# Kernel tuning notes

Measured on AMD Instinct MI355X. Metric: run time of the kernel, lower is better.

## Reference

```python
import jax, jax.numpy as jnp
import numpy as np

DIM = 512
CTX_DIM = 1024
NUM_HEADS = 8
HEAD_DIM = DIM // NUM_HEADS
SCALE = DIM ** (-0.5)  # module uses full dim, not head_dim


def setup_inputs() -> dict:
    key = jax.random.key(0)
    k1, k2, k3, k4, k5 = jax.random.split(key, 5)
    B, NQ, NK = 4, 1024, 2048
    q = jax.random.normal(k1, (B, NQ, DIM), dtype=jnp.float32)
    context = jax.random.normal(k2, (B, NK, CTX_DIM), dtype=jnp.float32)
    # Linear weights stored as [in, out] so projection is x @ W (no bias).
    Wq = jax.random.normal(k3, (DIM, DIM), dtype=jnp.float32) * (DIM ** -0.5)
    Wk = jax.random.normal(k4, (CTX_DIM, DIM), dtype=jnp.float32) * (CTX_DIM ** -0.5)
    Wv = jax.random.normal(k5, (CTX_DIM, DIM), dtype=jnp.float32) * (CTX_DIM ** -0.5)
    return {"q": q, "context": context, "Wq": Wq, "Wk": Wk, "Wv": Wv}


def reference(q, context, Wq, Wk, Wv):
    B, NQ, _ = q.shape
    # Projections
    qh = (q @ Wq).reshape(B, NQ, NUM_HEADS, HEAD_DIM)          # [B,Nq,H,D]
    kh = (context @ Wk).reshape(B, -1, NUM_HEADS, HEAD_DIM)     # [B,Nk,H,D]
    vh = (context @ Wv).reshape(B, -1, NUM_HEADS, HEAD_DIM)     # [B,Nk,H,D]
    # Scores and softmax (dropout is identity in eval / reference mode)
    attn_scores = jnp.einsum("bqhd,bkhd->bhqk", qh, kh) * SCALE
    attn_weights = jax.nn.softmax(attn_scores, axis=-1)         # [B,H,Nq,Nk]
    # Weighted sum of values, merge heads back
    ctx = jnp.einsum("bhqk,bkhd->bqhd", attn_weights, vh)
    context_vec = ctx.reshape(B, NQ, NUM_HEADS * HEAD_DIM)      # [B,Nq,dim]
    return context_vec, attn_weights
```

## Files before the change

### kernel.cpp

```cpp
#include <hip/hip_runtime.h>
#include <hip/hip_bf16.h>

#define B_ 4
#define NQ_ 1024
#define NK_ 2048
#define DIM_ 512
#define CTX_ 1024
#define NH_ 8
#define HD_ 64
static constexpr float SCALE_ = 0.04419417382415922f;

typedef short bf16x8 __attribute__((ext_vector_type(8)));
typedef float f32x4 __attribute__((ext_vector_type(4)));

__device__ __forceinline__ unsigned f2u(float f) { union { float f; unsigned u; } v; v.f = f; return v.u; }

__device__ __forceinline__ bf16x8 pack8(float4 lo, float4 hi) {
  union { unsigned u[4]; bf16x8 v; } r;
  r.u[0] = __builtin_amdgcn_perm(f2u(lo.y), f2u(lo.x), 0x07060302u);
  r.u[1] = __builtin_amdgcn_perm(f2u(lo.w), f2u(lo.z), 0x07060302u);
  r.u[2] = __builtin_amdgcn_perm(f2u(hi.y), f2u(hi.x), 0x07060302u);
  r.u[3] = __builtin_amdgcn_perm(f2u(hi.w), f2u(hi.z), 0x07060302u);
  return r.v;
}

__device__ __forceinline__ unsigned short f2bf_rne(float f) {
  unsigned u = f2u(f);
  u += 0x7fffu + ((u >> 16) & 1u);
  return (unsigned short)(u >> 16);
}

__global__ __launch_bounds__(256) void transpose_w(
    const float* __restrict__ Wq, const float* __restrict__ Wk,
    const float* __restrict__ Wv, unsigned short* __restrict__ Wt) {
  int mat = blockIdx.z;
  const float* W; unsigned short* T; int K;
  if (mat == 0)      { W = Wq; T = Wt;                         K = DIM_; }
  else if (mat == 1) { W = Wk; T = Wt + DIM_*DIM_;             K = CTX_; }
  else               { W = Wv; T = Wt + DIM_*DIM_ + DIM_*CTX_; K = CTX_; }
  int k0 = blockIdx.x * 64;
  if (k0 >= K) return;
  int n0 = blockIdx.y * 64;
  __shared__ unsigned short tl[64][64];
  int tid = threadIdx.x;
  {
    int nb = (tid & 15) * 4;
    int rbase = tid >> 4;
    #pragma unroll
    for (int p = 0; p < 4; ++p) {
      int kr = rbase + p * 16;
      float4 v = *(const float4*)(W + (size_t)(k0 + kr) * DIM_ + n0 + nb);
      int ck = kr >> 3, ko = kr & 7;
      tl[nb + 0][((ck ^ ((nb + 0) & 7)) << 3) | ko] = (unsigned short)(f2u(v.x) >> 16);
      tl[nb + 1][((ck ^ ((nb + 1) & 7)) << 3) | ko] = (unsigned short)(f2u(v.y) >> 16);
      tl[nb + 2][((ck ^ ((nb + 2) & 7)) << 3) | ko] = (unsigned short)(f2u(v.z) >> 16);
      tl[nb + 3][((ck ^ ((nb + 3) & 7)) << 3) | ko] = (unsigned short)(f2u(v.w) >> 16);
    }
  }
  __syncthreads();
  {
    int nr = tid >> 2, cc = tid & 3;
    #pragma unroll
    for (int p = 0; p < 2; ++p) {
      int c = cc + p * 4;
      bf16x8 v = *(const bf16x8*)&tl[nr][(c ^ (nr & 7)) << 3];
      *(bf16x8*)(T + (size_t)(n0 + nr) * K + k0 + c * 8) = v;
    }
  }
}

template<int TRANS>
__global__ __launch_bounds__(256) void gemm_proj(
    const float* __restrict__ A, const unsigned short* __restrict__ Wt,
    unsigned short* __restrict__ C, int M, int K) {
  int tid = threadIdx.x, lane = tid & 63, wid = tid >> 6;
  int m0 = blockIdx.x * 128 + (wid >> 1) * 64;
  int n0 = blockIdx.y * 128 + (wid & 1) * 64;
  int rl = lane & 15, ch = (lane >> 4) * 8;
  const float* aptr = A + (size_t)(m0 + rl) * K + ch;
  const unsigned short* bptr = Wt + (size_t)(n0 + rl) * K + ch;
  f32x4 acc[4][4] = {};
  for (int k0 = 0; k0 < K; k0 += 32) {
    bf16x8 af[4], bfr[4];
    #pragma unroll
    for (int i = 0; i < 4; ++i) {
      const float* p = aptr + (size_t)i * 16 * K + k0;
      float4 lo = *(const float4*)p;
      float4 hi = *(const float4*)(p + 4);
      af[i] = pack8(lo, hi);
    }
    #pragma unroll
    for (int j = 0; j < 4; ++j)
      bfr[j] = *(const bf16x8*)(bptr + (size_t)j * 16 * K + k0);
    #pragma unroll
    for (int i = 0; i < 4; ++i)
      #pragma unroll
      for (int j = 0; j < 4; ++j)
        acc[i][j] = __builtin_amdgcn_mfma_f32_16x16x32_bf16(af[i], bfr[j], acc[i][j], 0, 0, 0);
  }
  int rq = (lane >> 4) * 4, cn = lane & 15;
  #pragma unroll
  for (int i = 0; i < 4; ++i)
    #pragma unroll
    for (int j = 0; j < 4; ++j)
      #pragma unroll
      for (int r = 0; r < 4; ++r) {
        int row = m0 + i * 16 + rq + r;
        int col = n0 + j * 16 + cn;
        unsigned short v = f2bf_rne(acc[i][j][r]);
        if (TRANS) {
          int b = row >> 11, k = row & 2047;
          int h = col >> 6, d = col & 63;
          C[((size_t)(b * NH_ + h) * HD_ + d) * NK_ + k] = v;
        } else {
          C[(size_t)row * DIM_ + col] = v;
        }
      }
}

__global__ __launch_bounds__(256) void attn_fwd(
    const unsigned short* __restrict__ Qh, const unsigned short* __restrict__ Kh,
    const unsigned short* __restrict__ Vt, float* __restrict__ outO,
    float* __restrict__ outW) {
  int bid = blockIdx.x;
  int qt = bid & 15, h = (bid >> 4) & 7, b = bid >> 7;
  int tid = threadIdx.x, lane = tid & 63, wid = tid >> 6;
  int q0 = qt * 64 + wid * 16;
  int rl = lane & 15, ch = (lane >> 4) * 8, rq = (lane >> 4) * 4;
  __shared__ unsigned short Plds[4][16][40];

  const unsigned short* qbase = Qh + (size_t)(b * NQ_ + q0 + rl) * DIM_ + h * HD_;
  bf16x8 aq0 = *(const bf16x8*)(qbase + ch);
  bf16x8 aq1 = *(const bf16x8*)(qbase + 32 + ch);

  const unsigned short* kbase = Kh + (size_t)(b * NK_ + rl) * DIM_ + h * HD_;

  float ps[4] = {0.f, 0.f, 0.f, 0.f};
  #pragma unroll 4
  for (int kt = 0; kt < NK_ / 16; ++kt) {
    const unsigned short* kp = kbase + (size_t)kt * 16 * DIM_;
    bf16x8 bk0 = *(const bf16x8*)(kp + ch);
    bf16x8 bk1 = *(const bf16x8*)(kp + 32 + ch);
    f32x4 s = {};
    s = __builtin_amdgcn_mfma_f32_16x16x32_bf16(aq0, bk0, s, 0, 0, 0);
    s = __builtin_amdgcn_mfma_f32_16x16x32_bf16(aq1, bk1, s, 0, 0, 0);
    #pragma unroll
    for (int r = 0; r < 4; ++r) ps[r] += __expf(s[r] * SCALE_);
  }
  #pragma unroll
  for (int m = 1; m < 16; m <<= 1)
    #pragma unroll
    for (int r = 0; r < 4; ++r) ps[r] += __shfl_xor(ps[r], m);
  float inv[4];
  #pragma unroll
  for (int r = 0; r < 4; ++r) inv[r] = 1.0f / ps[r];

  f32x4 accO[4] = {};
  float* wbase = outW + (size_t)((b * NH_ + h) * NQ_ + q0 + rq) * NK_;
  for (int kc = 0; kc < NK_ / 32; ++kc) {
    #pragma unroll
    for (int t = 0; t < 2; ++t) {
      int kt = kc * 2 + t;
      const unsigned short* kp = kbase + (size_t)kt * 16 * DIM_;
      bf16x8 bk0 = *(const bf16x8*)(kp + ch);
      bf16x8 bk1 = *(const bf16x8*)(kp + 32 + ch);
      f32x4 s = {};
      s = __builtin_amdgcn_mfma_f32_16x16x32_bf16(aq0, bk0, s, 0, 0, 0);
      s = __builtin_amdgcn_mfma_f32_16x16x32_bf16(aq1, bk1, s, 0, 0, 0);
      #pragma unroll
      for (int r = 0; r < 4; ++r) {
        float p = __expf(s[r] * SCALE_) * inv[r];
        wbase[(size_t)r * NK_ + kt * 16 + rl] = p;
        Plds[wid][rq + r][t * 16 + rl] = (unsigned short)(f2u(p) >> 16);
      }
    }
    bf16x8 ap = *(const bf16x8*)&Plds[wid][rl][ch];
    #pragma unroll
    for (int dt = 0; dt < 4; ++dt) {
      const unsigned short* vp =
          Vt + ((size_t)(b * NH_ + h) * HD_ + dt * 16 + rl) * NK_ + kc * 32 + ch;
      bf16x8 bv = *(const bf16x8*)vp;
      accO[dt] = __builtin_amdgcn_mfma_f32_16x16x32_bf16(ap, bv, accO[dt], 0, 0, 0);
    }
  }
  float* obase = outO + (size_t)(b * NQ_ + q0 + rq) * DIM_ + h * HD_;
  #pragma unroll
  for (int dt = 0; dt < 4; ++dt)
    #pragma unroll
    for (int r = 0; r < 4; ++r)
      obase[(size_t)r * DIM_ + dt * 16 + rl] = accO[dt][r];
}

extern "C" void kernel_launch(void* const* d_in, const int* in_sizes, int n_in,
                              void* d_out, int out_size, void* d_ws, size_t ws_size,
                              hipStream_t stream) {
  (void)in_sizes; (void)n_in; (void)out_size; (void)ws_size;
  const float* q   = (const float*)d_in[0];
  const float* ctx = (const float*)d_in[1];
  const float* Wq  = (const float*)d_in[2];
  const float* Wk  = (const float*)d_in[3];
  const float* Wv  = (const float*)d_in[4];

  unsigned short* Wt = (unsigned short*)d_ws;
  unsigned short* Qh = Wt + 1310720;
  unsigned short* Kh = Qh + 2097152;
  unsigned short* Vt = Kh + 4194304;
  float* outO = (float*)d_out;
  float* outW = outO + (size_t)B_ * NQ_ * DIM_;

  transpose_w<<<dim3(16, 8, 3), 256, 0, stream>>>(Wq, Wk, Wv, Wt);
  gemm_proj<0><<<dim3(32, 4), 256, 0, stream>>>(q,   Wt,                  Qh, 4096, DIM_);
  gemm_proj<0><<<dim3(64, 4), 256, 0, stream>>>(ctx, Wt + 262144,         Kh, 8192, CTX_);
  gemm_proj<1><<<dim3(64, 4), 256, 0, stream>>>(ctx, Wt + 262144 + 524288, Vt, 8192, CTX_);
  attn_fwd<<<dim3(512), 256, 0, stream>>>(Qh, Kh, Vt, outO, outW);
}
```

Baseline: 564.5 us.

## Fuse K and V projections into one GEMM and shrink projection tiles

Replaces the templated projection GEMM with a Q-only kernel and a fused K/V kernel. The fused kernel reads each context fragment once and feeds both the Wk and Wv MFMAs, removing one full pass over the fp32 context tensor. Tiles shrink from 128x128 to 64x64 per block, which raises the block count for better CU occupancy but lowers per-wave operand reuse. The transposed V store stays scattered.

```diff
diff --git a/kernel.cpp b/kernel.cpp
--- a/kernel.cpp
+++ b/kernel.cpp
@@ -69,53 +69,72 @@
   }
 }
 
-template<int TRANS>
-__global__ __launch_bounds__(256) void gemm_proj(
+__global__ __launch_bounds__(256) void gemm_q(
     const float* __restrict__ A, const unsigned short* __restrict__ Wt,
-    unsigned short* __restrict__ C, int M, int K) {
+    unsigned short* __restrict__ C) {
   int tid = threadIdx.x, lane = tid & 63, wid = tid >> 6;
-  int m0 = blockIdx.x * 128 + (wid >> 1) * 64;
-  int n0 = blockIdx.y * 128 + (wid & 1) * 64;
+  int m0 = blockIdx.x * 64 + wid * 16;
+  int n0 = blockIdx.y * 64;
   int rl = lane & 15, ch = (lane >> 4) * 8;
-  const float* aptr = A + (size_t)(m0 + rl) * K + ch;
-  const unsigned short* bptr = Wt + (size_t)(n0 + rl) * K + ch;
-  f32x4 acc[4][4] = {};
-  for (int k0 = 0; k0 < K; k0 += 32) {
-    bf16x8 af[4], bfr[4];
-    #pragma unroll
-    for (int i = 0; i < 4; ++i) {
-      const float* p = aptr + (size_t)i * 16 * K + k0;
-      float4 lo = *(const float4*)p;
-      float4 hi = *(const float4*)(p + 4);
-      af[i] = pack8(lo, hi);
-    }
-    #pragma unroll
-    for (int j = 0; j < 4; ++j)
-      bfr[j] = *(const bf16x8*)(bptr + (size_t)j * 16 * K + k0);
-    #pragma unroll
-    for (int i = 0; i < 4; ++i)
-      #pragma unroll
-      for (int j = 0; j < 4; ++j)
-        acc[i][j] = __builtin_amdgcn_mfma_f32_16x16x32_bf16(af[i], bfr[j], acc[i][j], 0, 0, 0);
-  }
-  int rq = (lane >> 4) * 4, cn = lane & 15;
-  #pragma unroll
-  for (int i = 0; i < 4; ++i)
-    #pragma unroll
-    for (int j = 0; j < 4; ++j)
-      #pragma unroll
-      for (int r = 0; r < 4; ++r) {
-        int row = m0 + i * 16 + rq + r;
-        int col = n0 + j * 16 + cn;
-        unsigned short v = f2bf_rne(acc[i][j][r]);
-        if (TRANS) {
-          int b = row >> 11, k = row & 2047;
-          int h = col >> 6, d = col & 63;
-          C[((size_t)(b * NH_ + h) * HD_ + d) * NK_ + k] = v;
-        } else {
-          C[(size_t)row * DIM_ + col] = v;
-        }
-      }
+  const float* aptr = A + (size_t)(m0 + rl) * DIM_ + ch;
+  const unsigned short* bptr = Wt + (size_t)(n0 + rl) * DIM_ + ch;
+  f32x4 acc[4] = {};
+  #pragma unroll 4
+  for (int k0 = 0; k0 < DIM_; k0 += 32) {
+    float4 lo = *(const float4*)(aptr + k0);
+    float4 hi = *(const float4*)(aptr + k0 + 4);
+    bf16x8 af = pack8(lo, hi);
+    #pragma unroll
+    for (int j = 0; j < 4; ++j) {
+      bf16x8 bfr = *(const bf16x8*)(bptr + (size_t)j * 16 * DIM_ + k0);
+      acc[j] = __builtin_amdgcn_mfma_f32_16x16x32_bf16(af, bfr, acc[j], 0, 0, 0);
+    }
+  }
+  int rq = (lane >> 4) * 4;
+  #pragma unroll
+  for (int j = 0; j < 4; ++j)
+    #pragma unroll
+    for (int r = 0; r < 4; ++r)
+      C[(size_t)(m0 + rq + r) * DIM_ + n0 + j * 16 + rl] = f2bf_rne(acc[j][r]);
+}
+
+__global__ __launch_bounds__(256) void gemm_kv(
+    const float* __restrict__ A, const unsigned short* __restrict__ Wtk,
+    const unsigned short* __restrict__ Wtv, unsigned short* __restrict__ Kh,
+    unsigned short* __restrict__ Vt) {
+  int tid = threadIdx.x, lane = tid & 63, wid = tid >> 6;
+  int m0 = blockIdx.x * 64 + wid * 16;
+  int n0 = blockIdx.y * 64;
+  int rl = lane & 15, ch = (lane >> 4) * 8;
+  const float* aptr = A + (size_t)(m0 + rl) * CTX_ + ch;
+  const unsigned short* bkp = Wtk + (size_t)(n0 + rl) * CTX_ + ch;
+  const unsigned short* bvp = Wtv + (size_t)(n0 + rl) * CTX_ + ch;
+  f32x4 accK[4] = {}, accV[4] = {};
+  #pragma unroll 2
+  for (int k0 = 0; k0 < CTX_; k0 += 32) {
+    float4 lo = *(const float4*)(aptr + k0);
+    float4 hi = *(const float4*)(aptr + k0 + 4);
+    bf16x8 af = pack8(lo, hi);
+    #pragma unroll
+    for (int j = 0; j < 4; ++j) {
+      bf16x8 bk = *(const bf16x8*)(bkp + (size_t)j * 16 * CTX_ + k0);
+      accK[j] = __builtin_amdgcn_mfma_f32_16x16x32_bf16(af, bk, accK[j], 0, 0, 0);
+      bf16x8 bv = *(const bf16x8*)(bvp + (size_t)j * 16 * CTX_ + k0);
+      accV[j] = __builtin_amdgcn_mfma_f32_16x16x32_bf16(af, bv, accV[j], 0, 0, 0);
+    }
+  }
+  int rq = (lane >> 4) * 4;
+  #pragma unroll
+  for (int j = 0; j < 4; ++j)
+    #pragma unroll
+    for (int r = 0; r < 4; ++r) {
+      int row = m0 + rq + r;
+      int col = n0 + j * 16 + rl;
+      Kh[(size_t)row * DIM_ + col] = f2bf_rne(accK[j][r]);
+      int b = row >> 11, kk = row & 2047;
+      int h = col >> 6, d = col & 63;
+      Vt[((size_t)(b * NH_ + h) * HD_ + d) * NK_ + kk] = f2bf_rne(accV[j][r]);
+    }
 }
 
 __global__ __launch_bounds__(256) void attn_fwd(
@@ -209,8 +228,7 @@
   float* outW = outO + (size_t)B_ * NQ_ * DIM_;
 
   transpose_w<<<dim3(16, 8, 3), 256, 0, stream>>>(Wq, Wk, Wv, Wt);
-  gemm_proj<0><<<dim3(32, 4), 256, 0, stream>>>(q,   Wt,                  Qh, 4096, DIM_);
-  gemm_proj<0><<<dim3(64, 4), 256, 0, stream>>>(ctx, Wt + 262144,         Kh, 8192, CTX_);
-  gemm_proj<1><<<dim3(64, 4), 256, 0, stream>>>(ctx, Wt + 262144 + 524288, Vt, 8192, CTX_);
+  gemm_q<<<dim3(64, 8), 256, 0, stream>>>(q, Wt, Qh);
+  gemm_kv<<<dim3(128, 8), 256, 0, stream>>>(ctx, Wt + 262144, Wt + 786432, Kh, Vt);
   attn_fwd<<<dim3(512), 256, 0, stream>>>(Qh, Kh, Vt, outO, outW);
 }
```

Result: slower. 615.0 us (+8.9%).

## Split attention denominator and main pass across key chunks for more parallelism

Applied to the files above, without the earlier changes.

Moves the softmax-denominator pass into its own kernel, which launches many small blocks over query tiles and key chunks, followed by a reduction kernel. The main pass splits the key dimension across the four waves of each block, writes partial outputs to workspace, and sums them in a combine kernel. A fused fallback is used when the workspace is too small. The aim is to fill the GPU better than the original 512-block launch, at the cost of extra launches and partial-output traffic.

```diff
diff --git a/kernel.cpp b/kernel.cpp
--- a/kernel.cpp
+++ b/kernel.cpp
@@ -118,26 +118,24 @@
       }
 }
 
-__global__ __launch_bounds__(256) void attn_fwd(
+__global__ __launch_bounds__(256) void attn_denom(
     const unsigned short* __restrict__ Qh, const unsigned short* __restrict__ Kh,
-    const unsigned short* __restrict__ Vt, float* __restrict__ outO,
-    float* __restrict__ outW) {
+    float* __restrict__ dnm_part) {
   int bid = blockIdx.x;
-  int qt = bid & 15, h = (bid >> 4) & 7, b = bid >> 7;
+  int kchi = bid & 3, qt = (bid >> 2) & 63, h = (bid >> 8) & 7, b = bid >> 11;
   int tid = threadIdx.x, lane = tid & 63, wid = tid >> 6;
-  int q0 = qt * 64 + wid * 16;
+  int kc = kchi * 4 + wid;
+  int q0 = qt * 16;
   int rl = lane & 15, ch = (lane >> 4) * 8, rq = (lane >> 4) * 4;
-  __shared__ unsigned short Plds[4][16][40];
 
   const unsigned short* qbase = Qh + (size_t)(b * NQ_ + q0 + rl) * DIM_ + h * HD_;
   bf16x8 aq0 = *(const bf16x8*)(qbase + ch);
   bf16x8 aq1 = *(const bf16x8*)(qbase + 32 + ch);
 
-  const unsigned short* kbase = Kh + (size_t)(b * NK_ + rl) * DIM_ + h * HD_;
-
+  const unsigned short* kbase = Kh + (size_t)(b * NK_ + kc * 128 + rl) * DIM_ + h * HD_;
   float ps[4] = {0.f, 0.f, 0.f, 0.f};
-  #pragma unroll 4
-  for (int kt = 0; kt < NK_ / 16; ++kt) {
+  #pragma unroll
+  for (int kt = 0; kt < 8; ++kt) {
     const unsigned short* kp = kbase + (size_t)kt * 16 * DIM_;
     bf16x8 bk0 = *(const bf16x8*)(kp + ch);
     bf16x8 bk1 = *(const bf16x8*)(kp + 32 + ch);
@@ -151,13 +149,51 @@
   for (int m = 1; m < 16; m <<= 1)
     #pragma unroll
     for (int r = 0; r < 4; ++r) ps[r] += __shfl_xor(ps[r], m);
+  if (rl == 0) {
+    #pragma unroll
+    for (int r = 0; r < 4; ++r)
+      dnm_part[((size_t)(b * NH_ + h) * 16 + kc) * NQ_ + q0 + rq + r] = ps[r];
+  }
+}
+
+__global__ __launch_bounds__(256) void dnm_reduce(
+    const float* __restrict__ dnm_part, float* __restrict__ dnm_inv) {
+  int i = blockIdx.x * 256 + threadIdx.x;
+  int bh = i >> 10, q = i & 1023;
+  float s = 0.f;
+  #pragma unroll
+  for (int kc = 0; kc < 16; ++kc)
+    s += dnm_part[((size_t)bh * 16 + kc) * NQ_ + q];
+  dnm_inv[i] = 1.0f / s;
+}
+
+__global__ __launch_bounds__(256) void attn_main_split(
+    const unsigned short* __restrict__ Qh, const unsigned short* __restrict__ Kh,
+    const unsigned short* __restrict__ Vt, const float* __restrict__ dnm_inv,
+    float* __restrict__ outW, float* __restrict__ O_part) {
+  int bid = blockIdx.x;
+  int qt = bid & 63, h = (bid >> 6) & 7, b = bid >> 9;
+  int tid = threadIdx.x, lane = tid & 63, wid = tid >> 6;
+  int ks = wid;
+  int q0 = qt * 16;
+  int rl = lane & 15, ch = (lane >> 4) * 8, rq = (lane >> 4) * 4;
+  __shared__ unsigned short Plds[4][16][40];
+
+  const unsigned short* qbase = Qh + (size_t)(b * NQ_ + q0 + rl) * DIM_ + h * HD_;
+  bf16x8 aq0 = *(const bf16x8*)(qbase + ch);
+  bf16x8 aq1 = *(const bf16x8*)(qbase + 32 + ch);
+
+  const unsigned short* kbase = Kh + (size_t)(b * NK_ + ks * 512 + rl) * DIM_ + h * HD_;
+
   float inv[4];
-  #pragma unroll
-  for (int r = 0; r < 4; ++r) inv[r] = 1.0f / ps[r];
+  const float* dbase = dnm_inv + (size_t)(b * NH_ + h) * NQ_ + q0 + rq;
+  #pragma unroll
+  for (int r = 0; r < 4; ++r) inv[r] = dbase[r];
 
   f32x4 accO[4] = {};
-  float* wbase = outW + (size_t)((b * NH_ + h) * NQ_ + q0 + rq) * NK_;
-  for (int kc = 0; kc < NK_ / 32; ++kc) {
+  float* wbase = outW + (size_t)((b * NH_ + h) * NQ_ + q0 + rq) * NK_ + ks * 512;
+  const unsigned short* vbase = Vt + ((size_t)(b * NH_ + h) * HD_ + rl) * NK_ + ks * 512;
+  for (int kc = 0; kc < 16; ++kc) {
     #pragma unroll
     for (int t = 0; t < 2; ++t) {
       int kt = kc * 2 + t;
@@ -177,6 +213,78 @@
     bf16x8 ap = *(const bf16x8*)&Plds[wid][rl][ch];
     #pragma unroll
     for (int dt = 0; dt < 4; ++dt) {
+      bf16x8 bv = *(const bf16x8*)(vbase + (size_t)dt * 16 * NK_ + kc * 32 + ch);
+      accO[dt] = __builtin_amdgcn_mfma_f32_16x16x32_bf16(ap, bv, accO[dt], 0, 0, 0);
+    }
+  }
+  float* obase = O_part + (size_t)ks * (B_ * NQ_ * DIM_) +
+                 (size_t)(b * NQ_ + q0 + rq) * DIM_ + h * HD_;
+  #pragma unroll
+  for (int dt = 0; dt < 4; ++dt)
+    #pragma unroll
+    for (int r = 0; r < 4; ++r)
+      obase[(size_t)r * DIM_ + dt * 16 + rl] = accO[dt][r];
+}
+
+__global__ __launch_bounds__(256) void o_combine(
+    const float* __restrict__ O_part, float* __restrict__ outO) {
+  size_t i = ((size_t)blockIdx.x * 256 + threadIdx.x) * 4;
+  const size_t S = (size_t)B_ * NQ_ * DIM_;
+  float4 a0 = *(const float4*)(O_part + i);
+  float4 a1 = *(const float4*)(O_part + S + i);
+  float4 a2 = *(const float4*)(O_part + 2 * S + i);
+  float4 a3 = *(const float4*)(O_part + 3 * S + i);
+  float4 o;
+  o.x = a0.x + a1.x + a2.x + a3.x;
+  o.y = a0.y + a1.y + a2.y + a3.y;
+  o.z = a0.z + a1.z + a2.z + a3.z;
+  o.w = a0.w + a1.w + a2.w + a3.w;
+  *(float4*)(outO + i) = o;
+}
+
+__global__ __launch_bounds__(256) void attn_main_fused(
+    const unsigned short* __restrict__ Qh, const unsigned short* __restrict__ Kh,
+    const unsigned short* __restrict__ Vt, const float* __restrict__ dnm_inv,
+    float* __restrict__ outO, float* __restrict__ outW) {
+  int bid = blockIdx.x;
+  int qt = bid & 15, h = (bid >> 4) & 7, b = bid >> 7;
+  int tid = threadIdx.x, lane = tid & 63, wid = tid >> 6;
+  int q0 = qt * 64 + wid * 16;
+  int rl = lane & 15, ch = (lane >> 4) * 8, rq = (lane >> 4) * 4;
+  __shared__ unsigned short Plds[4][16][40];
+
+  const unsigned short* qbase = Qh + (size_t)(b * NQ_ + q0 + rl) * DIM_ + h * HD_;
+  bf16x8 aq0 = *(const bf16x8*)(qbase + ch);
+  bf16x8 aq1 = *(const bf16x8*)(qbase + 32 + ch);
+  const unsigned short* kbase = Kh + (size_t)(b * NK_ + rl) * DIM_ + h * HD_;
+
+  float inv[4];
+  const float* dbase = dnm_inv + (size_t)(b * NH_ + h) * NQ_ + q0 + rq;
+  #pragma unroll
+  for (int r = 0; r < 4; ++r) inv[r] = dbase[r];
+
+  f32x4 accO[4] = {};
+  float* wbase = outW + (size_t)((b * NH_ + h) * NQ_ + q0 + rq) * NK_;
+  for (int kc = 0; kc < NK_ / 32; ++kc) {
+    #pragma unroll
+    for (int t = 0; t < 2; ++t) {
+      int kt = kc * 2 + t;
+      const unsigned short* kp = kbase + (size_t)kt * 16 * DIM_;
+      bf16x8 bk0 = *(const bf16x8*)(kp + ch);
+      bf16x8 bk1 = *(const bf16x8*)(kp + 32 + ch);
+      f32x4 s = {};
+      s = __builtin_amdgcn_mfma_f32_16x16x32_bf16(aq0, bk0, s, 0, 0, 0);
+      s = __builtin_amdgcn_mfma_f32_16x16x32_bf16(aq1, bk1, s, 0, 0, 0);
+      #pragma unroll
+      for (int r = 0; r < 4; ++r) {
+        float p = __expf(s[r] * SCALE_) * inv[r];
+        wbase[(size_t)r * NK_ + kt * 16 + rl] = p;
+        Plds[wid][rq + r][t * 16 + rl] = (unsigned short)(f2u(p) >> 16);
+      }
+    }
+    bf16x8 ap = *(const bf16x8*)&Plds[wid][rl][ch];
+    #pragma unroll
+    for (int dt = 0; dt < 4; ++dt) {
       const unsigned short* vp =
           Vt + ((size_t)(b * NH_ + h) * HD_ + dt * 16 + rl) * NK_ + kc * 32 + ch;
       bf16x8 bv = *(const bf16x8*)vp;
@@ -194,7 +302,7 @@
 extern "C" void kernel_launch(void* const* d_in, const int* in_sizes, int n_in,
                               void* d_out, int out_size, void* d_ws, size_t ws_size,
                               hipStream_t stream) {
-  (void)in_sizes; (void)n_in; (void)out_size; (void)ws_size;
+  (void)in_sizes; (void)n_in; (void)out_size;
   const float* q   = (const float*)d_in[0];
   const float* ctx = (const float*)d_in[1];
   const float* Wq  = (const float*)d_in[2];
@@ -205,12 +313,27 @@
   unsigned short* Qh = Wt + 1310720;
   unsigned short* Kh = Qh + 2097152;
   unsigned short* Vt = Kh + 4194304;
+  const size_t staging_bytes = 23592960;
+  float* dnm_part = (float*)((char*)d_ws + staging_bytes);
+  float* dnm_inv  = dnm_part + 524288;
+  float* O_part   = dnm_inv + 32768;
+  const size_t need_split = staging_bytes + (524288ull + 32768 + 8388608) * 4;
+
   float* outO = (float*)d_out;
   float* outW = outO + (size_t)B_ * NQ_ * DIM_;
 
   transpose_w<<<dim3(16, 8, 3), 256, 0, stream>>>(Wq, Wk, Wv, Wt);
-  gemm_proj<0><<<dim3(32, 4), 256, 0, stream>>>(q,   Wt,                  Qh, 4096, DIM_);
-  gemm_proj<0><<<dim3(64, 4), 256, 0, stream>>>(ctx, Wt + 262144,         Kh, 8192, CTX_);
+  gemm_proj<0><<<dim3(32, 4), 256, 0, stream>>>(q,   Wt,                   Qh, 4096, DIM_);
+  gemm_proj<0><<<dim3(64, 4), 256, 0, stream>>>(ctx, Wt + 262144,          Kh, 8192, CTX_);
   gemm_proj<1><<<dim3(64, 4), 256, 0, stream>>>(ctx, Wt + 262144 + 524288, Vt, 8192, CTX_);
-  attn_fwd<<<dim3(512), 256, 0, stream>>>(Qh, Kh, Vt, outO, outW);
-}
+
+  attn_denom<<<dim3(8192), 256, 0, stream>>>(Qh, Kh, dnm_part);
+  dnm_reduce<<<dim3(128), 256, 0, stream>>>(dnm_part, dnm_inv);
+
+  if (ws_size >= need_split) {
+    attn_main_split<<<dim3(2048), 256, 0, stream>>>(Qh, Kh, Vt, dnm_inv, outW, O_part);
+    o_combine<<<dim3(2048), 256, 0, stream>>>(O_part, outO);
+  } else {
+    attn_main_fused<<<dim3(512), 256, 0, stream>>>(Qh, Kh, Vt, dnm_inv, outO, outW);
+  }
+}
```

New measurement: 588.3 us. +4.2%, slower.
